# Optimization experiments

Measured on AMD Instinct MI355X. Metric: run time of the kernel, lower is better.

The kernel has to match this reference:

```python
import jax, jax.numpy as jnp
import numpy as np

B, D, E, H, OUT = 4096, 1024, 8, 4096, 1024


def setup_inputs() -> dict:
    key = jax.random.key(0)
    ks = jax.random.split(key, 8)
    s_in = 1.0 / np.sqrt(D)
    s_h = 1.0 / np.sqrt(H)
    return {
        "x": jax.random.normal(ks[0], (B, D), dtype=jnp.float32),
        "Wg": jax.random.uniform(ks[1], (D, E), minval=-s_in, maxval=s_in, dtype=jnp.float32),
        "bg": jnp.zeros((E,), dtype=jnp.float32),
        "W1": jax.random.uniform(ks[2], (E, D, H), minval=-s_in, maxval=s_in, dtype=jnp.float32),
        "b1": jnp.zeros((E, H), dtype=jnp.float32),
        "W2": jax.random.uniform(ks[3], (E, H, OUT), minval=-s_h, maxval=s_h, dtype=jnp.float32),
        "b2": jnp.zeros((E, OUT), dtype=jnp.float32),
        "w_bal": jnp.float32(0.01),
    }


def reference(x, Wg, bg, W1, b1, W2, b2, w_bal):
    # Gating: softmax then top-1 (== argmax of logits)
    gate_logits = x @ Wg + bg                      # [B, E]
    assign = jnp.argmax(gate_logits, axis=1)       # [B] top-1 expert
    onehot = jax.nn.one_hot(assign, E, dtype=x.dtype)  # [B, E] dispatch mask

    # Dense dispatch: run every expert MLP, combine by one-hot (top-1 select).
    # Original returns raw expert output (no gate-prob scaling).
    h = jax.nn.relu(jnp.einsum("bd,edh->ebh", x, W1) + b1[:, None, :])  # [E, B, H]
    y = jnp.einsum("ebh,eho->ebo", h, W2) + b2[:, None, :]              # [E, B, OUT]
    output = jnp.einsum("ebo,be->bo", y, onehot)                        # [B, OUT]

    # Load-balance loss on per-expert token counts
    loads = onehot.sum(axis=0)                     # [E]
    balance_loss = jnp.sum((loads - loads.mean()) ** 2) / E
    return output, balance_loss * w_bal
```

## Files before the change

### kernel.cpp

```cpp
#include <hip/hip_runtime.h>
#include <hip/hip_bf16.h>

typedef unsigned short u16;
typedef __attribute__((ext_vector_type(8))) short bf16x8;
typedef __attribute__((ext_vector_type(4))) float f32x4;

#define BTOK 4096
#define DDIM 1024
#define NEXP 8
#define HDIM 4096
#define ODIM 1024
#define MAXTILES 40
#define MAXROWS (MAXTILES * 128)

__device__ __forceinline__ u16 f2bf(float f) {
  unsigned u = __float_as_uint(f);
  return (u16)((u + 0x7FFFu + ((u >> 16) & 1u)) >> 16);
}
__device__ __forceinline__ u16 cvt_bf(float f) {
  __hip_bfloat16 h = __float2bfloat16(f);
  u16 r;
  __builtin_memcpy(&r, &h, 2);
  return r;
}

__device__ __forceinline__ void gload16(const void* g, void* l) {
  __builtin_amdgcn_global_load_lds(
      (const __attribute__((address_space(1))) void*)g,
      (__attribute__((address_space(3))) void*)l, 16, 0, 0);
}

__global__ __launch_bounds__(256) void init_kernel(int* __restrict__ ctrl,
                                                   int* __restrict__ rowmap) {
  int i = blockIdx.x * 256 + threadIdx.x;
  if (i < 1024)
    ctrl[i] = 0;
  else
    rowmap[i - 1024] = -1;
}

__global__ __launch_bounds__(256) void gate_kernel(
    const float* __restrict__ x, const float* __restrict__ Wg,
    const float* __restrict__ bg, int* __restrict__ assign,
    int* __restrict__ counts) {
  int wave = threadIdx.x >> 6;
  int lane = threadIdx.x & 63;
  int b = blockIdx.x * 4 + wave;
  const float* xr = x + (size_t)b * DDIM;
  double acc[NEXP];
#pragma unroll
  for (int e = 0; e < NEXP; ++e) acc[e] = 0.0;
  for (int d = lane; d < DDIM; d += 64) {
    float xv = xr[d];
    const float4* wrow = (const float4*)(Wg + d * NEXP);
    float4 w0 = wrow[0], w1 = wrow[1];
    acc[0] += (double)xv * (double)w0.x;
    acc[1] += (double)xv * (double)w0.y;
    acc[2] += (double)xv * (double)w0.z;
    acc[3] += (double)xv * (double)w0.w;
    acc[4] += (double)xv * (double)w1.x;
    acc[5] += (double)xv * (double)w1.y;
    acc[6] += (double)xv * (double)w1.z;
    acc[7] += (double)xv * (double)w1.w;
  }
#pragma unroll
  for (int e = 0; e < NEXP; ++e) {
    double v = acc[e];
#pragma unroll
    for (int off = 32; off > 0; off >>= 1) v += __shfl_xor(v, off);
    acc[e] = v;
  }
  if (lane == 0) {
    int best = 0;
    double bv = acc[0] + (double)bg[0];
#pragma unroll
    for (int e = 1; e < NEXP; ++e) {
      double v = acc[e] + (double)bg[e];
      if (v > bv) { bv = v; best = e; }
    }
    assign[b] = best;
    atomicAdd(&counts[best], 1);
  }
}

__global__ void setup_kernel(const int* __restrict__ counts,
                             const float* __restrict__ wbal,
                             int* __restrict__ offp, int* __restrict__ tile_e,
                             int* __restrict__ tile_m, int* __restrict__ meta,
                             float* __restrict__ loss_out) {
  if (threadIdx.x != 0 || blockIdx.x != 0) return;
  int off = 0, nt = 0;
  for (int e = 0; e < NEXP; ++e) {
    offp[e] = off;
    int pc = (counts[e] + 127) & ~127;
    for (int t = 0; t < (pc >> 7); ++t) {
      tile_e[nt] = e;
      tile_m[nt] = off + t * 128;
      ++nt;
    }
    off += pc;
  }
  offp[NEXP] = off;
  meta[0] = nt;
  float mean = (float)BTOK / (float)NEXP;
  float s = 0.f;
  for (int e = 0; e < NEXP; ++e) {
    float d = (float)counts[e] - mean;
    s += d * d;
  }
  loss_out[0] = s / (float)NEXP * wbal[0];
}

__global__ __launch_bounds__(256) void gather_kernel(
    const float* __restrict__ x, const int* __restrict__ assign,
    const int* __restrict__ offp, int* __restrict__ fill,
    int* __restrict__ rowmap, u16* __restrict__ xg) {
  int b = blockIdx.x;
  __shared__ int srow;
  if (threadIdx.x == 0) {
    int e = assign[b];
    int pos = atomicAdd(&fill[e], 1);
    int row = offp[e] + pos;
    rowmap[row] = b;
    srow = row;
  }
  __syncthreads();
  int row = srow;
  float4 v = *(const float4*)(x + (size_t)b * DDIM + threadIdx.x * 4);
  ushort4 o;
  o.x = f2bf(v.x);
  o.y = f2bf(v.y);
  o.z = f2bf(v.z);
  o.w = f2bf(v.w);
  *(ushort4*)(xg + (size_t)row * DDIM + threadIdx.x * 4) = o;
}

__global__ __launch_bounds__(256) void transpose_conv(
    const float* __restrict__ W, u16* __restrict__ wt, int inN,
    size_t estrideIn, int KR, int NC) {
  const int e = blockIdx.z;
  const int kb = blockIdx.x * 64, nb = blockIdx.y * 64;
  __shared__ __align__(16) float lds[64][68];
  const float* src = W + (size_t)e * estrideIn;
  const int t = threadIdx.x;
  const int rr = t >> 4, cc = (t & 15) * 4;
#pragma unroll
  for (int p = 0; p < 4; ++p) {
    float4 v =
        *(const float4*)(src + (size_t)(kb + rr + p * 16) * inN + nb + cc);
    *(float4*)&lds[rr + p * 16][cc] = v;
  }
  __syncthreads();
  const int n = t & 63, kg = (t >> 6) * 16;
  alignas(16) u16 tmp[16];
#pragma unroll
  for (int i = 0; i < 16; ++i) tmp[i] = cvt_bf(lds[kg + i][n]);
  u16* dst = wt + ((size_t)e * NC + nb + n) * KR + kb + kg;
  *(float4*)dst = *(float4*)&tmp[0];
  *(float4*)(dst + 8) = *(float4*)&tmp[8];
}

template <int MODE>
__device__ __forceinline__ void gemm_core(
    u16* lds, int bx, int by, int bz, const u16* __restrict__ A, int lda,
    const u16* __restrict__ BT, int ldb, int nbRows,
    const float* __restrict__ bias, const int* __restrict__ tile_e,
    const int* __restrict__ tile_m, u16* __restrict__ Hout, int ldn,
    float* __restrict__ P, size_t pStride, int nkt) {
  const int e = tile_e[bx];
  const int m0 = tile_m[bx];
  const int n0 = by * 128;
  const int kOff = bz * nkt * 32;

  const int tid = threadIdx.x;
  const int lane = tid & 63;
  const int wave = tid >> 6;
  const int wr = wave >> 1, wc = wave & 1;
  const int fr = lane & 15;
  const int kqr = lane >> 4;

  const int r0 = tid >> 2, k0 = (tid & 3) ^ ((r0 >> 1) & 3);
  const int r1 = (tid + 256) >> 2, k1 = ((tid + 256) & 3) ^ ((r1 >> 1) & 3);
  const u16* aS0 = A + (size_t)(m0 + r0) * lda + kOff + k0 * 8;
  const u16* aS1 = A + (size_t)(m0 + r1) * lda + kOff + k1 * 8;
  const u16* bPan = BT + ((size_t)e * nbRows + n0) * ldb + kOff;
  const u16* bS0 = bPan + (size_t)r0 * ldb + k0 * 8;
  const u16* bS1 = bPan + (size_t)r1 * ldb + k1 * 8;
  const int dst0 = (tid & ~63) * 8;
  const int dst1 = dst0 + 2048;

  int aOff[4], bOff[4];
#pragma unroll
  for (int i = 0; i < 4; ++i) {
    int r = wr * 64 + i * 16 + fr;
    aOff[i] = (r * 4 + (kqr ^ ((r >> 1) & 3))) * 8;
    int c = wc * 64 + i * 16 + fr;
    bOff[i] = (c * 4 + (kqr ^ ((c >> 1) & 3))) * 8;
  }

  f32x4 acc[4][4];
#pragma unroll
  for (int i = 0; i < 4; ++i)
#pragma unroll
    for (int j = 0; j < 4; ++j)
#pragma unroll
      for (int r = 0; r < 4; ++r) acc[i][j][r] = 0.f;

  auto stage = [&](int buf, int kt) {
    const int ko = kt * 32;
    u16* base = lds + buf * 8192;
    gload16(aS0 + ko, base + dst0);
    gload16(aS1 + ko, base + dst1);
    gload16(bS0 + ko, base + 4096 + dst0);
    gload16(bS1 + ko, base + 4096 + dst1);
  };
  auto compute = [&](int buf) {
    const u16* base = lds + buf * 8192;
    bf16x8 af[4], bfr[4];
#pragma unroll
    for (int i = 0; i < 4; ++i) {
      af[i] = *(const bf16x8*)(base + aOff[i]);
      bfr[i] = *(const bf16x8*)(base + 4096 + bOff[i]);
    }
    __builtin_amdgcn_s_setprio(1);
#pragma unroll
    for (int i = 0; i < 4; ++i)
#pragma unroll
      for (int j = 0; j < 4; ++j)
        acc[i][j] = __builtin_amdgcn_mfma_f32_16x16x32_bf16(af[i], bfr[j],
                                                            acc[i][j], 0, 0, 0);
    __builtin_amdgcn_s_setprio(0);
  };

  stage(0, 0);
  stage(1, 1);
  __builtin_amdgcn_sched_barrier(0);
  asm volatile("s_waitcnt vmcnt(4)" ::: "memory");
  __builtin_amdgcn_s_barrier();
  __builtin_amdgcn_sched_barrier(0);

  int cur = 0, nst = 2;
#pragma unroll 1
  for (int t = 0; t < nkt; ++t) {
    const bool more = (t + 2 < nkt);
    if (more) stage(nst, t + 2);
    compute(cur);
    cur = (cur == 2) ? 0 : cur + 1;
    nst = (nst == 2) ? 0 : nst + 1;
    if (t + 1 < nkt) {
      __builtin_amdgcn_sched_barrier(0);
      if (more)
        asm volatile("s_waitcnt vmcnt(4)" ::: "memory");
      else
        asm volatile("s_waitcnt vmcnt(0)" ::: "memory");
      __builtin_amdgcn_s_barrier();
      __builtin_amdgcn_sched_barrier(0);
    }
  }

  if constexpr (MODE == 0) {
#pragma unroll
    for (int i = 0; i < 4; ++i) {
      int rbase = m0 + wr * 64 + i * 16 + (lane >> 4) * 4;
#pragma unroll
      for (int j = 0; j < 4; ++j) {
        int col = n0 + wc * 64 + j * 16 + fr;
        float bv = bias[e * ldn + col];
#pragma unroll
        for (int r = 0; r < 4; ++r) {
          float v = acc[i][j][r] + bv;
          v = v > 0.f ? v : 0.f;
          Hout[(size_t)(rbase + r) * ldn + col] = f2bf(v);
        }
      }
    }
  } else {
    float* Pp = P + bz * pStride;
#pragma unroll
    for (int i = 0; i < 4; ++i) {
      int rbase = m0 + wr * 64 + i * 16 + (lane >> 4) * 4;
#pragma unroll
      for (int j = 0; j < 4; ++j) {
        int col = n0 + wc * 64 + j * 16 + fr;
#pragma unroll
        for (int r = 0; r < 4; ++r)
          Pp[(size_t)(rbase + r) * ODIM + col] = acc[i][j][r];
      }
    }
  }
}

__global__ __launch_bounds__(256) void moe_gemm1(
    const u16* __restrict__ xg, const u16* __restrict__ wt1,
    const float* __restrict__ b1, const int* __restrict__ tile_e,
    const int* __restrict__ tile_m, const int* __restrict__ meta,
    u16* __restrict__ h) {
  __shared__ __align__(16) u16 lds[3 * 8192];
  const int orig = blockIdx.y * MAXTILES + blockIdx.x;
  const int xcd = orig & 7;
  const int idx = orig >> 3;
  const int bx = idx % MAXTILES;
  const int by = xcd * 4 + idx / MAXTILES;
  if (bx >= meta[0]) return;
  gemm_core<0>(lds, bx, by, 0, xg, DDIM, wt1, DDIM, HDIM, b1, tile_e, tile_m,
               h, HDIM, nullptr, 0, DDIM / 32);
}

__global__ __launch_bounds__(256) void moe_gemm2(
    const u16* __restrict__ h, const u16* __restrict__ wt2,
    const int* __restrict__ tile_e, const int* __restrict__ tile_m,
    const int* __restrict__ meta, float* __restrict__ P, size_t pStride) {
  __shared__ __align__(16) u16 lds[3 * 8192];
  const int orig = blockIdx.y * MAXTILES + blockIdx.x;
  const int xcd = orig & 7;
  const int idx = orig >> 3;
  const int bx = idx;
  const int by = xcd;
  if (bx >= meta[0]) return;
  gemm_core<1>(lds, bx, by, blockIdx.z, h, HDIM, wt2, HDIM, ODIM, nullptr,
               tile_e, tile_m, nullptr, 0, P, pStride, (HDIM / 2) / 32);
}

__global__ __launch_bounds__(256) void reduce_kernel(
    const float* __restrict__ P, size_t pStride, const int* __restrict__ rowmap,
    const int* __restrict__ tile_e, const int* __restrict__ tile_m,
    const int* __restrict__ meta, const float* __restrict__ b2,
    float* __restrict__ out) {
  if ((int)blockIdx.x >= meta[0]) return;
  const int e = tile_e[blockIdx.x];
  const int m0 = tile_m[blockIdx.x];
  const int c0 = blockIdx.y * 128;
#pragma unroll 1
  for (int it = 0; it < 16; ++it) {
    int idx = it * 256 + threadIdx.x;
    int r = idx >> 5, cq = idx & 31;
    int row = m0 + r;
    int tok = rowmap[row];
    if (tok < 0) continue;
    int c = c0 + cq * 4;
    float4 a = *(const float4*)(P + (size_t)row * ODIM + c);
    float4 b = *(const float4*)(P + pStride + (size_t)row * ODIM + c);
    float4 bb = *(const float4*)(b2 + (size_t)e * ODIM + c);
    float4 o;
    o.x = a.x + b.x + bb.x;
    o.y = a.y + b.y + bb.y;
    o.z = a.z + b.z + bb.z;
    o.w = a.w + b.w + bb.w;
    *(float4*)(out + (size_t)tok * ODIM + c) = o;
  }
}

extern "C" void kernel_launch(void* const* d_in, const int* in_sizes, int n_in,
                              void* d_out, int out_size, void* d_ws,
                              size_t ws_size, hipStream_t stream) {
  const float* x = (const float*)d_in[0];
  const float* Wg = (const float*)d_in[1];
  const float* bg = (const float*)d_in[2];
  const float* W1 = (const float*)d_in[3];
  const float* b1 = (const float*)d_in[4];
  const float* W2 = (const float*)d_in[5];
  const float* b2 = (const float*)d_in[6];
  const float* wbal = (const float*)d_in[7];
  float* out = (float*)d_out;

  char* ws = (char*)d_ws;
  int* counts = (int*)(ws + 0);
  int* fill = (int*)(ws + 64);
  int* offp = (int*)(ws + 128);
  int* meta = (int*)(ws + 192);
  int* tile_e = (int*)(ws + 256);
  int* tile_m = (int*)(ws + 512);
  int* assign = (int*)(ws + 4096);
  int* rowmap = (int*)(ws + 20480);
  u16* xg = (u16*)(ws + 65536);
  u16* h = (u16*)(ws + 10551296);
  float* P = (float*)(ws + 52494336);
  u16* wt1 = (u16*)(ws + 94437376);
  u16* wt2 = (u16*)(ws + 161546240);
  const size_t pStride = (size_t)MAXROWS * ODIM;

  init_kernel<<<24, 256, 0, stream>>>((int*)ws, rowmap);
  gate_kernel<<<BTOK / 4, 256, 0, stream>>>(x, Wg, bg, assign, counts);
  setup_kernel<<<1, 64, 0, stream>>>(counts, wbal, offp, tile_e, tile_m, meta,
                                     out + (size_t)BTOK * ODIM);
  gather_kernel<<<BTOK, 256, 0, stream>>>(x, assign, offp, fill, rowmap, xg);

  transpose_conv<<<dim3(DDIM / 64, HDIM / 64, NEXP), 256, 0, stream>>>(
      W1, wt1, HDIM, (size_t)DDIM * HDIM, DDIM, HDIM);
  transpose_conv<<<dim3(HDIM / 64, ODIM / 64, NEXP), 256, 0, stream>>>(
      W2, wt2, ODIM, (size_t)HDIM * ODIM, HDIM, ODIM);

  moe_gemm1<<<dim3(MAXTILES, HDIM / 128), 256, 0, stream>>>(
      xg, wt1, b1, tile_e, tile_m, meta, h);
  moe_gemm2<<<dim3(MAXTILES, ODIM / 128, 2), 256, 0, stream>>>(
      h, wt2, tile_e, tile_m, meta, P, pStride);
  reduce_kernel<<<dim3(MAXTILES, ODIM / 128), 256, 0, stream>>>(
      P, pStride, rowmap, tile_e, tile_m, meta, b2, out);
}
```

Baseline: 361.9 us.

## Enlarge MoE GEMM row tiles to 256 with 512-thread blocks

Doubles the GEMM M-tile from 128 to 256 rows and runs each block with 8 waves instead of 4. A is staged in two 256-row loads and B in one 128-row load per k-step, so each weight panel feeds twice as many token rows. This cuts the repeated weight reads from global memory and the number of tiles. Expert padding now rounds to 256 rows, which adds wasted rows for small experts, and the larger 72KB LDS footprint per block may limit occupancy. The weight transpose-convert kernel also moves to 128-wide k tiles so each thread writes 64 bytes.

```diff
diff --git a/kernel.cpp b/kernel.cpp
--- a/kernel.cpp
+++ b/kernel.cpp
@@ -10,8 +10,8 @@
 #define NEXP 8
 #define HDIM 4096
 #define ODIM 1024
-#define MAXTILES 40
-#define MAXROWS (MAXTILES * 128)
+#define MAXT 23
+#define MROWS (MAXT * 256)
 
 __device__ __forceinline__ u16 f2bf(float f) {
   unsigned u = __float_as_uint(f);
@@ -92,10 +92,10 @@
   int off = 0, nt = 0;
   for (int e = 0; e < NEXP; ++e) {
     offp[e] = off;
-    int pc = (counts[e] + 127) & ~127;
-    for (int t = 0; t < (pc >> 7); ++t) {
+    int pc = (counts[e] + 255) & ~255;
+    for (int t = 0; t < (pc >> 8); ++t) {
       tile_e[nt] = e;
-      tile_m[nt] = off + t * 128;
+      tile_m[nt] = off + t * 256;
       ++nt;
     }
     off += pc;
@@ -136,28 +136,29 @@
 }
 
 __global__ __launch_bounds__(256) void transpose_conv(
-    const float* __restrict__ W, u16* __restrict__ wt, int inN,
-    size_t estrideIn, int KR, int NC) {
+    const float* __restrict__ W, u16* __restrict__ wt, int N, int K) {
   const int e = blockIdx.z;
-  const int kb = blockIdx.x * 64, nb = blockIdx.y * 64;
-  __shared__ __align__(16) float lds[64][68];
-  const float* src = W + (size_t)e * estrideIn;
+  const int kb = blockIdx.x * 128, nb = blockIdx.y * 64;
+  __shared__ __align__(16) float lds[128][68];
+  const float* src = W + (size_t)e * K * N;
   const int t = threadIdx.x;
   const int rr = t >> 4, cc = (t & 15) * 4;
 #pragma unroll
-  for (int p = 0; p < 4; ++p) {
+  for (int p = 0; p < 8; ++p) {
     float4 v =
-        *(const float4*)(src + (size_t)(kb + rr + p * 16) * inN + nb + cc);
+        *(const float4*)(src + (size_t)(kb + rr + p * 16) * N + nb + cc);
     *(float4*)&lds[rr + p * 16][cc] = v;
   }
   __syncthreads();
-  const int n = t & 63, kg = (t >> 6) * 16;
-  alignas(16) u16 tmp[16];
-#pragma unroll
-  for (int i = 0; i < 16; ++i) tmp[i] = cvt_bf(lds[kg + i][n]);
-  u16* dst = wt + ((size_t)e * NC + nb + n) * KR + kb + kg;
+  const int n = t & 63, ks = (t >> 6) * 32;
+  alignas(16) u16 tmp[32];
+#pragma unroll
+  for (int i = 0; i < 32; ++i) tmp[i] = cvt_bf(lds[ks + i][n]);
+  u16* dst = wt + ((size_t)e * N + nb + n) * K + kb + ks;
   *(float4*)dst = *(float4*)&tmp[0];
   *(float4*)(dst + 8) = *(float4*)&tmp[8];
+  *(float4*)(dst + 16) = *(float4*)&tmp[16];
+  *(float4*)(dst + 24) = *(float4*)&tmp[24];
 }
 
 template <int MODE>
@@ -180,14 +181,14 @@
   const int kqr = lane >> 4;
 
   const int r0 = tid >> 2, k0 = (tid & 3) ^ ((r0 >> 1) & 3);
-  const int r1 = (tid + 256) >> 2, k1 = ((tid + 256) & 3) ^ ((r1 >> 1) & 3);
+  const int r1 = (tid + 512) >> 2, k1 = ((tid + 512) & 3) ^ ((r1 >> 1) & 3);
   const u16* aS0 = A + (size_t)(m0 + r0) * lda + kOff + k0 * 8;
   const u16* aS1 = A + (size_t)(m0 + r1) * lda + kOff + k1 * 8;
   const u16* bPan = BT + ((size_t)e * nbRows + n0) * ldb + kOff;
   const u16* bS0 = bPan + (size_t)r0 * ldb + k0 * 8;
-  const u16* bS1 = bPan + (size_t)r1 * ldb + k1 * 8;
-  const int dst0 = (tid & ~63) * 8;
-  const int dst1 = dst0 + 2048;
+  const int dstA0 = (tid & ~63) * 8;
+  const int dstA1 = dstA0 + 512 * 8;
+  const int dstB = (tid & ~63) * 8;
 
   int aOff[4], bOff[4];
 #pragma unroll
@@ -195,7 +196,7 @@
     int r = wr * 64 + i * 16 + fr;
     aOff[i] = (r * 4 + (kqr ^ ((r >> 1) & 3))) * 8;
     int c = wc * 64 + i * 16 + fr;
-    bOff[i] = (c * 4 + (kqr ^ ((c >> 1) & 3))) * 8;
+    bOff[i] = 8192 + (c * 4 + (kqr ^ ((c >> 1) & 3))) * 8;
   }
 
   f32x4 acc[4][4];
@@ -208,19 +209,18 @@
 
   auto stage = [&](int buf, int kt) {
     const int ko = kt * 32;
-    u16* base = lds + buf * 8192;
-    gload16(aS0 + ko, base + dst0);
-    gload16(aS1 + ko, base + dst1);
-    gload16(bS0 + ko, base + 4096 + dst0);
-    gload16(bS1 + ko, base + 4096 + dst1);
+    u16* base = lds + buf * 12288;
+    gload16(aS0 + ko, base + dstA0);
+    gload16(aS1 + ko, base + dstA1);
+    gload16(bS0 + ko, base + 8192 + dstB);
   };
   auto compute = [&](int buf) {
-    const u16* base = lds + buf * 8192;
+    const u16* base = lds + buf * 12288;
     bf16x8 af[4], bfr[4];
 #pragma unroll
     for (int i = 0; i < 4; ++i) {
       af[i] = *(const bf16x8*)(base + aOff[i]);
-      bfr[i] = *(const bf16x8*)(base + 4096 + bOff[i]);
+      bfr[i] = *(const bf16x8*)(base + bOff[i]);
     }
     __builtin_amdgcn_s_setprio(1);
 #pragma unroll
@@ -235,7 +235,7 @@
   stage(0, 0);
   stage(1, 1);
   __builtin_amdgcn_sched_barrier(0);
-  asm volatile("s_waitcnt vmcnt(4)" ::: "memory");
+  asm volatile("s_waitcnt vmcnt(3)" ::: "memory");
   __builtin_amdgcn_s_barrier();
   __builtin_amdgcn_sched_barrier(0);
 
@@ -250,7 +250,7 @@
     if (t + 1 < nkt) {
       __builtin_amdgcn_sched_barrier(0);
       if (more)
-        asm volatile("s_waitcnt vmcnt(4)" ::: "memory");
+        asm volatile("s_waitcnt vmcnt(3)" ::: "memory");
       else
         asm volatile("s_waitcnt vmcnt(0)" ::: "memory");
       __builtin_amdgcn_s_barrier();
@@ -290,31 +290,31 @@
   }
 }
 
-__global__ __launch_bounds__(256) void moe_gemm1(
+__global__ __launch_bounds__(512, 4) void moe_gemm1(
     const u16* __restrict__ xg, const u16* __restrict__ wt1,
     const float* __restrict__ b1, const int* __restrict__ tile_e,
     const int* __restrict__ tile_m, const int* __restrict__ meta,
     u16* __restrict__ h) {
-  __shared__ __align__(16) u16 lds[3 * 8192];
-  const int orig = blockIdx.y * MAXTILES + blockIdx.x;
+  __shared__ __align__(16) u16 lds[3 * 12288];
+  const int orig = blockIdx.y * MAXT + blockIdx.x;
   const int xcd = orig & 7;
-  const int idx = orig >> 3;
-  const int bx = idx % MAXTILES;
-  const int by = xcd * 4 + idx / MAXTILES;
+  const int i = orig >> 3;
+  const int bx = i >> 2;
+  const int by = xcd * 4 + (i & 3);
   if (bx >= meta[0]) return;
   gemm_core<0>(lds, bx, by, 0, xg, DDIM, wt1, DDIM, HDIM, b1, tile_e, tile_m,
                h, HDIM, nullptr, 0, DDIM / 32);
 }
 
-__global__ __launch_bounds__(256) void moe_gemm2(
+__global__ __launch_bounds__(512, 4) void moe_gemm2(
     const u16* __restrict__ h, const u16* __restrict__ wt2,
     const int* __restrict__ tile_e, const int* __restrict__ tile_m,
     const int* __restrict__ meta, float* __restrict__ P, size_t pStride) {
-  __shared__ __align__(16) u16 lds[3 * 8192];
-  const int orig = blockIdx.y * MAXTILES + blockIdx.x;
+  __shared__ __align__(16) u16 lds[3 * 12288];
+  const int orig = blockIdx.y * MAXT + blockIdx.x;
   const int xcd = orig & 7;
-  const int idx = orig >> 3;
-  const int bx = idx;
+  const int i = orig >> 3;
+  const int bx = i;
   const int by = xcd;
   if (bx >= meta[0]) return;
   gemm_core<1>(lds, bx, by, blockIdx.z, h, HDIM, wt2, HDIM, ODIM, nullptr,
@@ -331,7 +331,7 @@
   const int m0 = tile_m[blockIdx.x];
   const int c0 = blockIdx.y * 128;
 #pragma unroll 1
-  for (int it = 0; it < 16; ++it) {
+  for (int it = 0; it < 32; ++it) {
     int idx = it * 256 + threadIdx.x;
     int r = idx >> 5, cq = idx & 31;
     int row = m0 + r;
@@ -373,27 +373,27 @@
   int* assign = (int*)(ws + 4096);
   int* rowmap = (int*)(ws + 20480);
   u16* xg = (u16*)(ws + 65536);
-  u16* h = (u16*)(ws + 10551296);
-  float* P = (float*)(ws + 52494336);
-  u16* wt1 = (u16*)(ws + 94437376);
-  u16* wt2 = (u16*)(ws + 161546240);
-  const size_t pStride = (size_t)MAXROWS * ODIM;
-
-  init_kernel<<<24, 256, 0, stream>>>((int*)ws, rowmap);
+  u16* h = (u16*)(ws + 12582912);
+  float* P = (float*)(ws + 61865984);
+  u16* wt1 = (u16*)(ws + 110100480);
+  u16* wt2 = (u16*)(ws + 177209344);
+  const size_t pStride = (size_t)MROWS * ODIM;
+
+  init_kernel<<<27, 256, 0, stream>>>((int*)ws, rowmap);
   gate_kernel<<<BTOK / 4, 256, 0, stream>>>(x, Wg, bg, assign, counts);
   setup_kernel<<<1, 64, 0, stream>>>(counts, wbal, offp, tile_e, tile_m, meta,
                                      out + (size_t)BTOK * ODIM);
   gather_kernel<<<BTOK, 256, 0, stream>>>(x, assign, offp, fill, rowmap, xg);
 
-  transpose_conv<<<dim3(DDIM / 64, HDIM / 64, NEXP), 256, 0, stream>>>(
-      W1, wt1, HDIM, (size_t)DDIM * HDIM, DDIM, HDIM);
-  transpose_conv<<<dim3(HDIM / 64, ODIM / 64, NEXP), 256, 0, stream>>>(
-      W2, wt2, ODIM, (size_t)HDIM * ODIM, HDIM, ODIM);
-
-  moe_gemm1<<<dim3(MAXTILES, HDIM / 128), 256, 0, stream>>>(
+  transpose_conv<<<dim3(DDIM / 128, HDIM / 64, NEXP), 256, 0, stream>>>(
+      W1, wt1, HDIM, DDIM);
+  transpose_conv<<<dim3(HDIM / 128, ODIM / 64, NEXP), 256, 0, stream>>>(
+      W2, wt2, ODIM, HDIM);
+
+  moe_gemm1<<<dim3(MAXT, HDIM / 128), 512, 0, stream>>>(
       xg, wt1, b1, tile_e, tile_m, meta, h);
-  moe_gemm2<<<dim3(MAXTILES, ODIM / 128, 2), 256, 0, stream>>>(
+  moe_gemm2<<<dim3(MAXT, ODIM / 128, 2), 512, 0, stream>>>(
       h, wt2, tile_e, tile_m, meta, P, pStride);
-  reduce_kernel<<<dim3(MAXTILES, ODIM / 128), 256, 0, stream>>>(
+  reduce_kernel<<<dim3(MAXT, ODIM / 128), 256, 0, stream>>>(
       P, pStride, rowmap, tile_e, tile_m, meta, b2, out);
 }
```

After: 374.9 us. 1.04x slower.
